# Performance work log

Measured on AMD Instinct MI355X. Metric: run time of the kernel, lower is better.

## Reference

```python
import jax, jax.numpy as jnp
import numpy as np

K = 7
PAD = K // 2
BN_EPS = 1e-5


def _unfold(x):
    # x: (B, C, H, W) -> (B, C, K*K, H, W), torch.F.unfold row-major kernel order
    B, C, H, W = x.shape
    xp = jnp.pad(x, ((0, 0), (0, 0), (PAD, PAD), (PAD, PAD)))
    patches = [xp[:, :, i:i + H, j:j + W] for i in range(K) for j in range(K)]
    return jnp.stack(patches, axis=2)


def setup_inputs() -> dict:
    key = jax.random.key(0)
    ks = jax.random.split(key, 6)
    B, C, H, W = 1, 256, 80, 80
    Cp = 19
    return {
        "x": jax.random.normal(ks[0], (B, C, H, W), jnp.float32),
        "coarse_probs": jax.random.uniform(ks[1], (B, Cp, H, W), jnp.float32),
        "sigma": jnp.ones((1,), jnp.float32),
        "w_feat": jax.random.normal(ks[2], (C, C), jnp.float32) * 0.05,
        "w_fuse": jax.random.normal(ks[3], (C, C), jnp.float32) * 0.05,
        "bn_gamma": jnp.ones((C,), jnp.float32),
        "bn_beta": jnp.zeros((C,), jnp.float32),
        "bn_mean": jax.random.normal(ks[4], (C,), jnp.float32) * 0.1,
        "bn_var": jax.random.uniform(ks[5], (C,), jnp.float32) + 0.5,
    }


def reference(x, coarse_probs, sigma, w_feat, w_fuse, bn_gamma, bn_beta, bn_mean, bn_var):
    # BatchNorm2d (inference, running stats)
    inv = jax.lax.rsqrt(bn_var + BN_EPS)
    xn = (x - bn_mean[None, :, None, None]) * (inv * bn_gamma)[None, :, None, None] \
         + bn_beta[None, :, None, None]

    # affinity from coarse probs over K*K neighborhood
    up = _unfold(coarse_probs)                      # (B, Cp, K2, H, W)
    center = up[:, :, (K * K - 1) // 2][:, :, None]  # (B, Cp, 1, H, W)
    dist_sq = jnp.sum((up - center) ** 2, axis=1)    # (B, K2, H, W)
    denom = 2.0 * jax.nn.relu(sigma[0]) ** 2 + 1e-8
    affinity = jax.nn.softmax(jnp.exp(-dist_sq / denom), axis=1)

    # feature_conv (1x1, no bias), unfold, weighted aggregation
    messages = jnp.einsum('oc,bchw->bohw', w_feat, xn)
    um = _unfold(messages)                           # (B, C, K2, H, W)
    agg = jnp.sum(um * affinity[:, None], axis=2)    # (B, C, H, W)

    refined = jnp.einsum('oc,bchw->bohw', w_fuse, agg)
    return x + refined
```

## Files before the change

### kernel.cpp

```cpp
#include <hip/hip_runtime.h>
#include <math.h>

#define HW_ 6400
#define C_ 256
#define CP_ 19

typedef __bf16 bf16x8 __attribute__((ext_vector_type(8)));
typedef float  f32x4  __attribute__((ext_vector_type(4)));

static __device__ __forceinline__ unsigned short f2bf(float f) {
    union { float f; unsigned int u; } x; x.f = f;
    unsigned int r = x.u + 0x7FFF + ((x.u >> 16) & 1);
    return (unsigned short)(r >> 16);
}
static __device__ __forceinline__ float bf2f(unsigned short u) {
    union { unsigned int ui; float fv; } cv;
    cv.ui = ((unsigned int)u) << 16;
    return cv.fv;
}

__global__ __launch_bounds__(256) void prep_kernel(
    const float* __restrict__ cp, const float* __restrict__ sigma,
    const float* __restrict__ wfeat, const float* __restrict__ wfuse,
    const float* __restrict__ g, const float* __restrict__ var,
    float* __restrict__ aff, float* __restrict__ S,
    unsigned short* __restrict__ WTb)
{
    if (blockIdx.x < 1600) {
        const int lane = threadIdx.x & 63;
        const int p = blockIdx.x * 4 + (threadIdx.x >> 6);
        const int h = p / 80, w = p - h * 80;
        const int k = (lane < 49) ? lane : 48;
        const int i = k / 7, j = k - i * 7;
        const int hh = h + i - 3, ww = w + j - 3;
        const bool ok = (hh >= 0) & (hh < 80) & (ww >= 0) & (ww < 80);
        const float msk = ok ? 1.0f : 0.0f;
        int q = hh * 80 + ww;
        q = min(max(q, 0), HW_ - 1);

        float s = fmaxf(sigma[0], 0.0f);
        float inv_denom = 1.0f / (2.0f * s * s + 1e-8f);

        float d = 0.0f;
#pragma unroll
        for (int c = 0; c < CP_; ++c) {
            float u = cp[c * HW_ + q];
            float ctr = __shfl(u, 24, 64);
            float t = u * msk - ctr;
            d += t * t;
        }
        float raw = __expf(-d * inv_denom);
        float e = (lane < 49) ? __expf(raw) : 0.0f;
        float einb = (ok && lane < 49) ? e : 0.0f;
        float sum = e, sumi = einb;
#pragma unroll
        for (int off = 32; off; off >>= 1) {
            sum  += __shfl_xor(sum,  off, 64);
            sumi += __shfl_xor(sumi, off, 64);
        }
        if (lane < 49) aff[k * HW_ + p] = e / sum;
        if (lane == 0) S[p] = sumi / sum;
    } else {
        __shared__ float sA[16][65];
        __shared__ float sB[16][64];
        const int tb = blockIdx.x - 1600;
        const int bm = (tb >> 2) * 64, bn = (tb & 3) * 64;
        const int t = threadIdx.x;
        const int arow = t >> 2, akc = (t & 3) * 4;
        const int bkr = t >> 4, bnc = (t & 15) * 4;
        const int ty = t >> 4, tx = t & 15;
        float acc[4][4] = {};
        for (int k0 = 0; k0 < C_; k0 += 16) {
            float4 a4 = *(const float4*)&wfuse[(bm + arow) * C_ + k0 + akc];
            sA[akc + 0][arow] = a4.x;
            sA[akc + 1][arow] = a4.y;
            sA[akc + 2][arow] = a4.z;
            sA[akc + 3][arow] = a4.w;
            *(float4*)&sB[bkr][bnc] = *(const float4*)&wfeat[(k0 + bkr) * C_ + bn + bnc];
            __syncthreads();
#pragma unroll
            for (int kk = 0; kk < 16; ++kk) {
                float a[4], b[4];
#pragma unroll
                for (int i = 0; i < 4; ++i) a[i] = sA[kk][ty * 4 + i];
                *(float4*)b = *(const float4*)&sB[kk][tx * 4];
#pragma unroll
                for (int i = 0; i < 4; ++i)
#pragma unroll
                    for (int j = 0; j < 4; ++j) acc[i][j] += a[i] * b[j];
            }
            __syncthreads();
        }
        const int cbase = bn + tx * 4;
        float sc[4];
#pragma unroll
        for (int j = 0; j < 4; ++j)
            sc[j] = g[cbase + j] * rsqrtf(var[cbase + j] + 1e-5f);
#pragma unroll
        for (int i = 0; i < 4; ++i) {
            const int o = bm + ty * 4 + i;
            unsigned int lo = (unsigned int)f2bf(acc[i][0] * sc[0]) |
                              ((unsigned int)f2bf(acc[i][1] * sc[1]) << 16);
            unsigned int hi = (unsigned int)f2bf(acc[i][2] * sc[2]) |
                              ((unsigned int)f2bf(acc[i][3] * sc[3]) << 16);
            *(uint2*)&WTb[o * C_ + cbase] = make_uint2(lo, hi);
        }
    }
}

__global__ __launch_bounds__(256) void agg_kernel(
    const float* __restrict__ x, const float* __restrict__ aff,
    const unsigned short* __restrict__ WTb,
    const float* __restrict__ g, const float* __restrict__ be,
    const float* __restrict__ mu, const float* __restrict__ var,
    unsigned short* __restrict__ aggT, float* __restrict__ wsum)
{
    if (blockIdx.x < 400) {
        const int b = blockIdx.x;
        const int pgt = b % 25, cht = b / 25;
        const int ch_l = threadIdx.x >> 5, pg_l = threadIdx.x & 31;
        const int pg = pgt * 32 + pg_l;
        const int p0 = pg * 8;
        const int h = pg / 10, w0 = (pg - (pg / 10) * 10) * 8;
        const int c0 = cht * 16 + ch_l;
        const float* xc0 = x + c0 * HW_;
        const float* xc1 = x + (c0 + 8) * HW_;

        float acc0[8] = {0.f, 0.f, 0.f, 0.f, 0.f, 0.f, 0.f, 0.f};
        float acc1[8] = {0.f, 0.f, 0.f, 0.f, 0.f, 0.f, 0.f, 0.f};

#pragma unroll
        for (int i = 0; i < 7; ++i) {
            int hh = h + i - 3;
            if (hh < 0 || hh >= 80) continue;
            float f0[16], f1[16];
            const int rb = hh * 80;
#pragma unroll
            for (int t = 0; t < 4; ++t) {
                int lin = rb + w0 - 4 + 4 * t;
                lin = min(max(lin, rb), rb + 76);
                *(float4*)&f0[4 * t] = *(const float4*)&xc0[lin];
                *(float4*)&f1[4 * t] = *(const float4*)&xc1[lin];
            }
#pragma unroll
            for (int e = 0; e < 16; ++e) {
                int col = w0 - 4 + e;
                bool okc = (col >= 0 && col < 80);
                f0[e] = okc ? f0[e] : 0.0f;
                f1[e] = okc ? f1[e] : 0.0f;
            }
#pragma unroll
            for (int j = 0; j < 7; ++j) {
                const int k = i * 7 + j;
                float av[8];
                *(float4*)&av[0] = *(const float4*)&aff[k * HW_ + p0];
                *(float4*)&av[4] = *(const float4*)&aff[k * HW_ + p0 + 4];
#pragma unroll
                for (int px = 0; px < 8; ++px) {
                    acc0[px] += av[px] * f0[px + j + 1];
                    acc1[px] += av[px] * f1[px + j + 1];
                }
            }
        }

        __shared__ float so[256][17];
#pragma unroll
        for (int px = 0; px < 8; ++px) {
            so[pg_l * 8 + px][ch_l]     = acc0[px];
            so[pg_l * 8 + px][ch_l + 8] = acc1[px];
        }
        __syncthreads();
        const int t = threadIdx.x;
        unsigned int pk[8];
#pragma unroll
        for (int d = 0; d < 8; ++d) {
            unsigned int lo = f2bf(so[t][2 * d]);
            unsigned int hi = f2bf(so[t][2 * d + 1]);
            pk[d] = lo | (hi << 16);
        }
        const int p = pgt * 256 + t;
        *(uint4*)&aggT[p * C_ + cht * 16]     = make_uint4(pk[0], pk[1], pk[2], pk[3]);
        *(uint4*)&aggT[p * C_ + cht * 16 + 8] = make_uint4(pk[4], pk[5], pk[6], pk[7]);
    } else {
        __shared__ float srL[C_];
        __shared__ float red[C_];
        const int t = threadIdx.x;
        {
            float scale = g[t] * rsqrtf(var[t] + 1e-5f);
            srL[t] = be[t] / scale - mu[t];
        }
        __syncthreads();
        const int o0 = (blockIdx.x - 400) * 64;
        const int r_l = t >> 2, seg = t & 3;
        const int row = o0 + r_l, c0 = seg * 64;
        float partial = 0.0f;
#pragma unroll
        for (int cc = 0; cc < 64; cc += 8) {
            unsigned short u8[8];
            *(uint4*)u8 = *(const uint4*)&WTb[row * C_ + c0 + cc];
#pragma unroll
            for (int e = 0; e < 8; ++e)
                partial += bf2f(u8[e]) * srL[c0 + cc + e];
        }
        red[t] = partial;
        __syncthreads();
        if (t < 64)
            wsum[o0 + t] = red[t * 4] + red[t * 4 + 1] + red[t * 4 + 2] + red[t * 4 + 3];
    }
}

__global__ __launch_bounds__(256) void mfma_gemm_kernel(
    const unsigned short* __restrict__ WTb, const unsigned short* __restrict__ aggT,
    const float* __restrict__ wsum, const float* __restrict__ S,
    const float* __restrict__ x, float* __restrict__ out)
{
    const int wave = threadIdx.x >> 6, lane = threadIdx.x & 63;
    const int q = lane >> 4, l15 = lane & 15;
    const int m0 = blockIdx.y * 128 + wave * 32;
    const int px0 = blockIdx.x * 64;

    f32x4 acc[2][4];
#pragma unroll
    for (int mi = 0; mi < 2; ++mi)
#pragma unroll
        for (int ni = 0; ni < 4; ++ni) acc[mi][ni] = (f32x4){0.f, 0.f, 0.f, 0.f};

#pragma unroll
    for (int k0 = 0; k0 < C_; k0 += 32) {
        bf16x8 af[2], bf[4];
#pragma unroll
        for (int mi = 0; mi < 2; ++mi)
            af[mi] = *(const bf16x8*)&WTb[(m0 + mi * 16 + l15) * C_ + k0 + q * 8];
#pragma unroll
        for (int ni = 0; ni < 4; ++ni)
            bf[ni] = *(const bf16x8*)&aggT[(px0 + ni * 16 + l15) * C_ + k0 + q * 8];
#pragma unroll
        for (int mi = 0; mi < 2; ++mi)
#pragma unroll
            for (int ni = 0; ni < 4; ++ni)
                acc[mi][ni] = __builtin_amdgcn_mfma_f32_16x16x32_bf16(
                    af[mi], bf[ni], acc[mi][ni], 0, 0, 0);
    }

#pragma unroll
    for (int mi = 0; mi < 2; ++mi) {
#pragma unroll
        for (int ni = 0; ni < 4; ++ni) {
            int p = px0 + ni * 16 + l15;
            float Sp = S[p];
#pragma unroll
            for (int r = 0; r < 4; ++r) {
                int m = m0 + mi * 16 + q * 4 + r;
                out[m * HW_ + p] = x[m * HW_ + p] + wsum[m] * Sp + acc[mi][ni][r];
            }
        }
    }
}

extern "C" void kernel_launch(void* const* d_in, const int* in_sizes, int n_in,
                              void* d_out, int out_size, void* d_ws, size_t ws_size,
                              hipStream_t stream) {
    const float* x      = (const float*)d_in[0];
    const float* cp     = (const float*)d_in[1];
    const float* sigma  = (const float*)d_in[2];
    const float* w_feat = (const float*)d_in[3];
    const float* w_fuse = (const float*)d_in[4];
    const float* g      = (const float*)d_in[5];
    const float* be     = (const float*)d_in[6];
    const float* mu     = (const float*)d_in[7];
    const float* var    = (const float*)d_in[8];
    float* out = (float*)d_out;

    char* wsb = (char*)d_ws;
    unsigned short* WTb  = (unsigned short*)wsb;
    unsigned short* aggT = (unsigned short*)(wsb + 131072);
    float* wsum = (float*)(wsb + 131072 + 3276800);
    float* S    = wsum + 256;
    float* aff  = S + HW_;

    prep_kernel<<<1616, 256, 0, stream>>>(cp, sigma, w_feat, w_fuse, g, var,
                                          aff, S, WTb);
    agg_kernel<<<404, 256, 0, stream>>>(x, aff, WTb, g, be, mu, var, aggT, wsum);
    mfma_gemm_kernel<<<dim3(100, 2), 256, 0, stream>>>(WTb, aggT, wsum, S, x, out);
}
```

Before: 128.4 us.

## Use MFMA for weight-product GEMM and halve pixels per thread in aggregation

The fp32 SIMT tiled GEMM that computes w_fuse·w_feat in the prep kernel is replaced by bf16 MFMA 16x16x32 instructions, with operands converted on the fly from global memory and no shared-memory staging. The aggregation kernel now gives each thread 4 pixels instead of 8 and launches twice as many blocks, aiming for more parallelism and lower register pressure at the cost of more redundant halo loads. The weight product now rounds its inputs to bf16 before multiplying, so precision drops slightly, and the B-operand loads are strided scalar reads.

After: 124.5 us. 1.03x faster.

```diff
diff --git a/kernel.cpp b/kernel.cpp
--- a/kernel.cpp
+++ b/kernel.cpp
@@ -18,6 +18,8 @@
     cv.ui = ((unsigned int)u) << 16;
     return cv.fv;
 }
+
+union bfpack { unsigned short u[8]; bf16x8 v; };
 
 __global__ __launch_bounds__(256) void prep_kernel(
     const float* __restrict__ cp, const float* __restrict__ sigma,
@@ -61,49 +63,45 @@
         if (lane < 49) aff[k * HW_ + p] = e / sum;
         if (lane == 0) S[p] = sumi / sum;
     } else {
-        __shared__ float sA[16][65];
-        __shared__ float sB[16][64];
         const int tb = blockIdx.x - 1600;
-        const int bm = (tb >> 2) * 64, bn = (tb & 3) * 64;
-        const int t = threadIdx.x;
-        const int arow = t >> 2, akc = (t & 3) * 4;
-        const int bkr = t >> 4, bnc = (t & 15) * 4;
-        const int ty = t >> 4, tx = t & 15;
-        float acc[4][4] = {};
-        for (int k0 = 0; k0 < C_; k0 += 16) {
-            float4 a4 = *(const float4*)&wfuse[(bm + arow) * C_ + k0 + akc];
-            sA[akc + 0][arow] = a4.x;
-            sA[akc + 1][arow] = a4.y;
-            sA[akc + 2][arow] = a4.z;
-            sA[akc + 3][arow] = a4.w;
-            *(float4*)&sB[bkr][bnc] = *(const float4*)&wfeat[(k0 + bkr) * C_ + bn + bnc];
-            __syncthreads();
-#pragma unroll
-            for (int kk = 0; kk < 16; ++kk) {
-                float a[4], b[4];
-#pragma unroll
-                for (int i = 0; i < 4; ++i) a[i] = sA[kk][ty * 4 + i];
-                *(float4*)b = *(const float4*)&sB[kk][tx * 4];
-#pragma unroll
-                for (int i = 0; i < 4; ++i)
-#pragma unroll
-                    for (int j = 0; j < 4; ++j) acc[i][j] += a[i] * b[j];
-            }
-            __syncthreads();
-        }
-        const int cbase = bn + tx * 4;
-        float sc[4];
-#pragma unroll
-        for (int j = 0; j < 4; ++j)
-            sc[j] = g[cbase + j] * rsqrtf(var[cbase + j] + 1e-5f);
-#pragma unroll
-        for (int i = 0; i < 4; ++i) {
-            const int o = bm + ty * 4 + i;
-            unsigned int lo = (unsigned int)f2bf(acc[i][0] * sc[0]) |
-                              ((unsigned int)f2bf(acc[i][1] * sc[1]) << 16);
-            unsigned int hi = (unsigned int)f2bf(acc[i][2] * sc[2]) |
-                              ((unsigned int)f2bf(acc[i][3] * sc[3]) << 16);
-            *(uint2*)&WTb[o * C_ + cbase] = make_uint2(lo, hi);
+        const int wv = threadIdx.x >> 6, lane = threadIdx.x & 63;
+        const int q = lane >> 4, l15 = lane & 15;
+        const int bo = (tb >> 2) * 64, bc = (tb & 3) * 64;
+        const int o0 = bo + wv * 16;
+
+        f32x4 acc[4];
+#pragma unroll
+        for (int nf = 0; nf < 4; ++nf) acc[nf] = (f32x4){0.f, 0.f, 0.f, 0.f};
+
+        for (int k0 = 0; k0 < C_; k0 += 32) {
+            bfpack ap;
+            {
+                const float* src = &wfuse[(o0 + l15) * C_ + k0 + q * 8];
+                float4 lo = *(const float4*)src;
+                float4 hi = *(const float4*)(src + 4);
+                ap.u[0] = f2bf(lo.x); ap.u[1] = f2bf(lo.y);
+                ap.u[2] = f2bf(lo.z); ap.u[3] = f2bf(lo.w);
+                ap.u[4] = f2bf(hi.x); ap.u[5] = f2bf(hi.y);
+                ap.u[6] = f2bf(hi.z); ap.u[7] = f2bf(hi.w);
+            }
+#pragma unroll
+            for (int nf = 0; nf < 4; ++nf) {
+                const int cB = bc + nf * 16 + l15;
+                bfpack bp;
+#pragma unroll
+                for (int j = 0; j < 8; ++j)
+                    bp.u[j] = f2bf(wfeat[(k0 + q * 8 + j) * C_ + cB]);
+                acc[nf] = __builtin_amdgcn_mfma_f32_16x16x32_bf16(
+                    ap.v, bp.v, acc[nf], 0, 0, 0);
+            }
+        }
+#pragma unroll
+        for (int nf = 0; nf < 4; ++nf) {
+            const int c = bc + nf * 16 + l15;
+            const float sc = g[c] * rsqrtf(var[c] + 1e-5f);
+#pragma unroll
+            for (int r = 0; r < 4; ++r)
+                WTb[(o0 + q * 4 + r) * C_ + c] = f2bf(acc[nf][r] * sc);
         }
     }
 }
@@ -115,35 +113,35 @@
     const float* __restrict__ mu, const float* __restrict__ var,
     unsigned short* __restrict__ aggT, float* __restrict__ wsum)
 {
-    if (blockIdx.x < 400) {
+    if (blockIdx.x < 800) {
         const int b = blockIdx.x;
-        const int pgt = b % 25, cht = b / 25;
+        const int pgt = b % 50, cht = b / 50;
         const int ch_l = threadIdx.x >> 5, pg_l = threadIdx.x & 31;
         const int pg = pgt * 32 + pg_l;
-        const int p0 = pg * 8;
-        const int h = pg / 10, w0 = (pg - (pg / 10) * 10) * 8;
+        const int p0 = pg * 4;
+        const int h = pg / 20, w0 = (pg - (pg / 20) * 20) * 4;
         const int c0 = cht * 16 + ch_l;
         const float* xc0 = x + c0 * HW_;
         const float* xc1 = x + (c0 + 8) * HW_;
 
-        float acc0[8] = {0.f, 0.f, 0.f, 0.f, 0.f, 0.f, 0.f, 0.f};
-        float acc1[8] = {0.f, 0.f, 0.f, 0.f, 0.f, 0.f, 0.f, 0.f};
+        float acc0[4] = {0.f, 0.f, 0.f, 0.f};
+        float acc1[4] = {0.f, 0.f, 0.f, 0.f};
 
 #pragma unroll
         for (int i = 0; i < 7; ++i) {
             int hh = h + i - 3;
             if (hh < 0 || hh >= 80) continue;
-            float f0[16], f1[16];
+            float f0[12], f1[12];
             const int rb = hh * 80;
 #pragma unroll
-            for (int t = 0; t < 4; ++t) {
+            for (int t = 0; t < 3; ++t) {
                 int lin = rb + w0 - 4 + 4 * t;
                 lin = min(max(lin, rb), rb + 76);
                 *(float4*)&f0[4 * t] = *(const float4*)&xc0[lin];
                 *(float4*)&f1[4 * t] = *(const float4*)&xc1[lin];
             }
 #pragma unroll
-            for (int e = 0; e < 16; ++e) {
+            for (int e = 0; e < 12; ++e) {
                 int col = w0 - 4 + e;
                 bool okc = (col >= 0 && col < 80);
                 f0[e] = okc ? f0[e] : 0.0f;
@@ -152,35 +150,35 @@
 #pragma unroll
             for (int j = 0; j < 7; ++j) {
                 const int k = i * 7 + j;
-                float av[8];
-                *(float4*)&av[0] = *(const float4*)&aff[k * HW_ + p0];
-                *(float4*)&av[4] = *(const float4*)&aff[k * HW_ + p0 + 4];
-#pragma unroll
-                for (int px = 0; px < 8; ++px) {
+                float av[4];
+                *(float4*)av = *(const float4*)&aff[k * HW_ + p0];
+#pragma unroll
+                for (int px = 0; px < 4; ++px) {
                     acc0[px] += av[px] * f0[px + j + 1];
                     acc1[px] += av[px] * f1[px + j + 1];
                 }
             }
         }
 
-        __shared__ float so[256][17];
-#pragma unroll
-        for (int px = 0; px < 8; ++px) {
-            so[pg_l * 8 + px][ch_l]     = acc0[px];
-            so[pg_l * 8 + px][ch_l + 8] = acc1[px];
+        __shared__ float so[128][17];
+#pragma unroll
+        for (int px = 0; px < 4; ++px) {
+            so[pg_l * 4 + px][ch_l]     = acc0[px];
+            so[pg_l * 4 + px][ch_l + 8] = acc1[px];
         }
         __syncthreads();
         const int t = threadIdx.x;
-        unsigned int pk[8];
-#pragma unroll
-        for (int d = 0; d < 8; ++d) {
-            unsigned int lo = f2bf(so[t][2 * d]);
-            unsigned int hi = f2bf(so[t][2 * d + 1]);
+        const int px_i = t >> 1, half = t & 1;
+        unsigned int pk[4];
+#pragma unroll
+        for (int d = 0; d < 4; ++d) {
+            unsigned int lo = f2bf(so[px_i][half * 8 + 2 * d]);
+            unsigned int hi = f2bf(so[px_i][half * 8 + 2 * d + 1]);
             pk[d] = lo | (hi << 16);
         }
-        const int p = pgt * 256 + t;
-        *(uint4*)&aggT[p * C_ + cht * 16]     = make_uint4(pk[0], pk[1], pk[2], pk[3]);
-        *(uint4*)&aggT[p * C_ + cht * 16 + 8] = make_uint4(pk[4], pk[5], pk[6], pk[7]);
+        const int p = pgt * 128 + px_i;
+        *(uint4*)&aggT[p * C_ + cht * 16 + half * 8] =
+            make_uint4(pk[0], pk[1], pk[2], pk[3]);
     } else {
         __shared__ float srL[C_];
         __shared__ float red[C_];
@@ -190,7 +188,7 @@
             srL[t] = be[t] / scale - mu[t];
         }
         __syncthreads();
-        const int o0 = (blockIdx.x - 400) * 64;
+        const int o0 = (blockIdx.x - 800) * 64;
         const int r_l = t >> 2, seg = t & 3;
         const int row = o0 + r_l, c0 = seg * 64;
         float partial = 0.0f;
@@ -280,6 +278,6 @@
 
     prep_kernel<<<1616, 256, 0, stream>>>(cp, sigma, w_feat, w_fuse, g, var,
                                           aff, S, WTb);
-    agg_kernel<<<404, 256, 0, stream>>>(x, aff, WTb, g, be, mu, var, aggT, wsum);
+    agg_kernel<<<804, 256, 0, stream>>>(x, aff, WTb, g, be, mu, var, aggT, wsum);
     mfma_gemm_kernel<<<dim3(100, 2), 256, 0, stream>>>(WTb, aggT, wsum, S, x, out);
 }
```
